# Kernel tuning notes

Hardware: AMD Instinct MI355X
Metric: run time of the kernel (lower is better)

## Reference

```python
import jax, jax.numpy as jnp
import numpy as np

CH = 256
HEADS = 4
RED = 8  # SE reduction on 2*CH channels


def _conv2d(x, w, pad):
    # x: [b,c,h,w], w: [o,i,kh,kw]
    return jax.lax.conv_general_dilated(
        x, w, window_strides=(1, 1), padding=[(pad, pad), (pad, pad)],
        dimension_numbers=('NCHW', 'OIHW', 'NCHW'))


def setup_inputs() -> dict:
    key = jax.random.key(0)
    ks = jax.random.split(key, 12)
    b, c, h, w = 4, CH, 64, 64
    c2 = 2 * c
    s = 0.02
    inp = {
        'color_feat': jax.random.normal(ks[0], (b, c, h, w), jnp.float32),
        'gray_feat': jax.random.normal(ks[1], (b, c, h, w), jnp.float32),
        'Wq': jax.random.normal(ks[2], (c, c), jnp.float32) * s,
        'Wk': jax.random.normal(ks[3], (c, c), jnp.float32) * s,
        'Wv': jax.random.normal(ks[4], (c, c), jnp.float32) * s,
        'Wproj': jax.random.normal(ks[5], (c, c), jnp.float32) * s,
        'ca_w1': jax.random.normal(ks[6], (c2 // RED, c2), jnp.float32) * s,
        'ca_w2': jax.random.normal(ks[7], (c2, c2 // RED), jnp.float32) * s,
        'sa_w': jax.random.normal(ks[8], (1, 2, 7, 7), jnp.float32) * s,
        'fuse_w': jax.random.normal(ks[9], (c, c2, 3, 3), jnp.float32) * s,
        'bn_gamma': jnp.ones((c,), jnp.float32),
        'bn_beta': jnp.zeros((c,), jnp.float32),
        'bn_mean': jnp.zeros((c,), jnp.float32),
        'bn_var': jnp.ones((c,), jnp.float32),
    }
    return inp


def reference(color_feat, gray_feat, Wq, Wk, Wv, Wproj, ca_w1, ca_w2,
              sa_w, fuse_w, bn_gamma, bn_beta, bn_mean, bn_var):
    b, c, h, w = color_feat.shape
    nh = HEADS
    d = c // nh
    scale = d ** -0.5

    def heads(x, W):
        # 1x1 conv then split heads: [b,c,h,w] -> [b,nh,hw,d]
        y = jnp.einsum('bchw,oc->bohw', x, W)
        return y.reshape(b, nh, d, h * w).transpose(0, 1, 3, 2)

    q = heads(color_feat, Wq)
    k = heads(gray_feat, Wk)
    v = heads(gray_feat, Wv)

    attn = jax.nn.softmax(jnp.einsum('bnid,bnjd->bnij', q, k) * scale, axis=-1)
    out = jnp.einsum('bnij,bnjd->bnid', attn, v)
    out = out.transpose(0, 1, 3, 2).reshape(b, c, h, w)
    out = jnp.einsum('bchw,oc->bohw', out, Wproj)

    cat = jnp.concatenate([out, gray_feat], axis=1)  # [b,2c,h,w]

    # Channel attention (SE with shared MLP on avg- and max-pooled vectors)
    def mlp(z):
        return jax.nn.relu(z @ ca_w1.T) @ ca_w2.T
    avg = cat.mean(axis=(2, 3))
    mx = cat.max(axis=(2, 3))
    wch = jax.nn.sigmoid(mlp(avg) + mlp(mx))[:, :, None, None]
    cat = cat * wch

    # Spatial attention: channel-mean/max -> 7x7 conv -> sigmoid gate
    sa_in = jnp.stack([cat.mean(axis=1), cat.max(axis=1)], axis=1)  # [b,2,h,w]
    wsp = jax.nn.sigmoid(_conv2d(sa_in, sa_w, pad=3))
    cat = cat * wsp

    # Fuse: 3x3 conv -> BatchNorm (inference stats) -> LeakyReLU(0.2)
    y = _conv2d(cat, fuse_w, pad=1)
    inv = bn_gamma / jnp.sqrt(bn_var + 1e-5)
    y = (y - bn_mean[None, :, None, None]) * inv[None, :, None, None] + bn_beta[None, :, None, None]
    return jnp.where(y > 0, y, 0.2 * y)
```

## Files before the change

### kernel.cpp

```cpp
#include <hip/hip_runtime.h>
#include <hip/hip_bf16.h>
#include <stdint.h>

#define HW_ 4096

typedef short bf16x8 __attribute__((ext_vector_type(8)));
typedef short short4v __attribute__((ext_vector_type(4)));
typedef short short8v __attribute__((ext_vector_type(8)));
typedef float f32x4 __attribute__((ext_vector_type(4)));
typedef float f32x16 __attribute__((ext_vector_type(16)));
typedef uint32_t u32x4 __attribute__((ext_vector_type(4)));

__device__ inline unsigned short f2bf(float x) {
  uint32_t u = __builtin_bit_cast(uint32_t, x);
  uint32_t r = ((u >> 16) & 1u) + 0x7fffu;
  return (unsigned short)((u + r) >> 16);
}
__device__ inline uint32_t cvt_pk_bf16(float lo, float hi) {
  uint32_t r;
  asm("v_cvt_pk_bf16_f32 %0, %1, %2" : "=v"(r) : "v"(lo), "v"(hi));
  return r;
}
__device__ inline float bf_lo(uint32_t u) { return __builtin_bit_cast(float, u << 16); }
__device__ inline float bf_hi(uint32_t u) { return __builtin_bit_cast(float, u & 0xffff0000u); }
__device__ inline void gld_lds16(const unsigned short* g, unsigned short* l) {
  __builtin_amdgcn_global_load_lds((const __attribute__((address_space(1))) void*)g,
                                   (__attribute__((address_space(3))) void*)l, 16, 0, 0);
}

__global__ __launch_bounds__(256) void xconv_kernel(
    const float* __restrict__ X, unsigned short* __restrict__ Y) {
  const int i = blockIdx.x * 256 + threadIdx.x;
  const int p = i & 4095;
  const int cg = (i >> 12) & 31;
  const int b = i >> 17;
  const float* src = X + ((size_t)b * 256 + cg * 8) * HW_ + p;
  float v[8];
#pragma unroll
  for (int e = 0; e < 8; ++e) v[e] = src[(size_t)e * HW_];
  uint4 o;
  o.x = cvt_pk_bf16(v[0], v[1]);
  o.y = cvt_pk_bf16(v[2], v[3]);
  o.z = cvt_pk_bf16(v[4], v[5]);
  o.w = cvt_pk_bf16(v[6], v[7]);
  *(uint4*)&Y[((size_t)(b * 32 + cg) * HW_ + p) * 8] = o;
}

__global__ __launch_bounds__(256) void prep_kernel(
    const float* __restrict__ Wq, const float* __restrict__ Wk,
    const float* __restrict__ Wv, const float* __restrict__ Wp,
    const float* __restrict__ fw,
    unsigned short* __restrict__ WqB, unsigned short* __restrict__ WkB,
    unsigned short* __restrict__ WvB, unsigned short* __restrict__ WpB,
    unsigned short* __restrict__ wt) {
  const int blk = blockIdx.x;
  if (blk < 128) {
    const int which = blk >> 5;
    const float* W = which == 0 ? Wq : which == 1 ? Wk : which == 2 ? Wv : Wp;
    unsigned short* Y = which == 0 ? WqB : which == 1 ? WkB : which == 2 ? WvB : WpB;
    const int i = (blk & 31) * 256 + threadIdx.x;
    const int o = i & 255;
    const int cg = i >> 8;
    float4 a = *(const float4*)&W[(size_t)o * 256 + cg * 8];
    float4 bq = *(const float4*)&W[(size_t)o * 256 + cg * 8 + 4];
    uint4 ov;
    ov.x = cvt_pk_bf16(a.x, a.y);
    ov.y = cvt_pk_bf16(a.z, a.w);
    ov.z = cvt_pk_bf16(bq.x, bq.y);
    ov.w = cvt_pk_bf16(bq.z, bq.w);
    *(uint4*)&Y[((size_t)cg * 256 + o) * 8] = ov;
  } else {
    const size_t i = (size_t)(blk - 128) * 256 + threadIdx.x;
    const int oc = (int)(i >> 9);
    const int ic = (int)(i & 511);
    const float* src = fw + i * 9;
#pragma unroll
    for (int tap = 0; tap < 9; ++tap)
      wt[((size_t)tap * 256 + oc) * 512 + ic] = f2bf(src[tap]);
  }
}

__global__ __launch_bounds__(256) void gemm_mfma_kernel(
    const unsigned short* __restrict__ Xbf, const unsigned short* __restrict__ Wbf,
    void* __restrict__ Yv, int mode, float oscale) {
  __shared__ unsigned short W_l[32][64][8];
  __shared__ unsigned short X_l[2][2][128][8];
  const int t = threadIdx.x;
  const int w = t >> 6;
  const int l = t & 63;
  const int n = l & 31;
  const int g32 = l >> 5;
  const int p0 = blockIdx.x * 128;
  const int o0 = blockIdx.y * 64;
  const int b = blockIdx.z;
  const int wo = w >> 1, wp = w & 1;
  const unsigned short* Xb = Xbf + (size_t)b * 32 * HW_ * 8;

  for (int i = t; i < 2048; i += 256) {
    const int ksg = i >> 6, oc = i & 63;
    gld_lds16(Wbf + ((size_t)ksg * 256 + o0 + oc) * 8, &W_l[0][0][0] + (size_t)i * 8);
  }
  {
    const int gg = t >> 7, pp = t & 127;
    gld_lds16(Xb + ((size_t)gg * HW_ + p0 + pp) * 8, &X_l[0][0][0][0] + (size_t)t * 8);
  }
  f32x16 acc[2] = {};
  int buf = 0;
  for (int ks = 0; ks < 16; ++ks) {
    asm volatile("s_waitcnt vmcnt(0)" ::: "memory");
    __syncthreads();
    if (ks < 15) {
      const int gg = t >> 7, pp = t & 127;
      gld_lds16(Xb + ((size_t)((ks + 1) * 2 + gg) * HW_ + p0 + pp) * 8,
                &X_l[buf ^ 1][0][0][0] + (size_t)t * 8);
    }
    bf16x8 af = *(const bf16x8*)&W_l[ks * 2 + g32][wo * 32 + n][0];
    bf16x8 b0 = *(const bf16x8*)&X_l[buf][g32][wp * 64 + n][0];
    bf16x8 b1 = *(const bf16x8*)&X_l[buf][g32][wp * 64 + 32 + n][0];
    acc[0] = __builtin_amdgcn_mfma_f32_32x32x16_bf16(af, b0, acc[0], 0, 0, 0);
    acc[1] = __builtin_amdgcn_mfma_f32_32x32x16_bf16(af, b1, acc[1], 0, 0, 0);
    buf ^= 1;
  }

  if (mode == 1) {
    unsigned short* Y = (unsigned short*)Yv;
    const size_t bh = (size_t)b * 4 + blockIdx.y;
#pragma unroll
    for (int pf = 0; pf < 2; ++pf) {
      const int p = p0 + wp * 64 + pf * 32 + n;
      unsigned short* dst = Y + (bh * HW_ + p) * 64 + wo * 32 + 4 * g32;
#pragma unroll
      for (int q = 0; q < 4; ++q) {
        uint2 uu;
        uu.x = cvt_pk_bf16(acc[pf][q * 4 + 0] * oscale, acc[pf][q * 4 + 1] * oscale);
        uu.y = cvt_pk_bf16(acc[pf][q * 4 + 2] * oscale, acc[pf][q * 4 + 3] * oscale);
        *(uint2*)&dst[8 * q] = uu;
      }
    }
  } else if (mode == 2) {
    unsigned short* Y = (unsigned short*)Yv;
#pragma unroll
    for (int pf = 0; pf < 2; ++pf) {
      const int p = p0 + wp * 64 + pf * 32 + n;
#pragma unroll
      for (int r = 0; r < 16; ++r) {
        const int m = (r & 3) + 8 * (r >> 2) + 4 * g32;
        Y[((size_t)b * 256 + o0 + wo * 32 + m) * HW_ + p] = f2bf(acc[pf][r]);
      }
    }
  } else {
    unsigned short* Y = (unsigned short*)Yv;
    const int cgb = (o0 + wo * 32) >> 3;
#pragma unroll
    for (int pf = 0; pf < 2; ++pf) {
      const int p = p0 + wp * 64 + pf * 32 + n;
#pragma unroll
      for (int q = 0; q < 4; ++q) {
        uint2 uu;
        uu.x = cvt_pk_bf16(acc[pf][q * 4 + 0], acc[pf][q * 4 + 1]);
        uu.y = cvt_pk_bf16(acc[pf][q * 4 + 2], acc[pf][q * 4 + 3]);
        *(uint2*)&Y[((size_t)(b * 32 + cgb + q) * HW_ + p) * 8 + 4 * g32] = uu;
      }
    }
  }
}

#define ATTN_STAGE(BUF, KP, VP)                                              \
  {                                                                          \
    gld_lds16((KP), &k_l[BUF][16 * w][0]);                                   \
    gld_lds16((KP) + (size_t)8 * 64, &k_l[BUF][16 * w + 8][0]);              \
    gld_lds16((VP), &v_l[BUF][16 * w][0]);                                   \
    gld_lds16((VP) + (size_t)8 * HW_, &v_l[BUF][16 * w + 8][0]);             \
  }

#define ATTN_COMPUTE(BUF)                                                    \
  {                                                                          \
    f32x4 accS[2][4];                                                        \
    _Pragma("unroll") for (int jt = 0; jt < 4; ++jt) {                       \
      const int jrow = jt * 16 + c;                                          \
      bf16x8 kf0 = *(const bf16x8*)&k_l[BUF][jrow][((0 + g) ^ (c & 7)) * 8]; \
      bf16x8 kf1 = *(const bf16x8*)&k_l[BUF][jrow][((4 + g) ^ (c & 7)) * 8]; \
      _Pragma("unroll") for (int qt = 0; qt < 2; ++qt) {                     \
        f32x4 s0 = __builtin_amdgcn_mfma_f32_16x16x32_bf16(kf0, qf[qt][0], zero4, 0, 0, 0); \
        accS[qt][jt] = __builtin_amdgcn_mfma_f32_16x16x32_bf16(kf1, qf[qt][1], s0, 0, 0, 0); \
      }                                                                      \
    }                                                                        \
    uint32_t pwu[2][2][4];                                                   \
    _Pragma("unroll") for (int qt = 0; qt < 2; ++qt) {                       \
      float rs = 0.f;                                                        \
      _Pragma("unroll") for (int jt = 0; jt < 4; ++jt) {                     \
        const float e0 = __builtin_amdgcn_exp2f(accS[qt][jt][0]);            \
        const float e1 = __builtin_amdgcn_exp2f(accS[qt][jt][1]);            \
        const float e2 = __builtin_amdgcn_exp2f(accS[qt][jt][2]);            \
        const float e3 = __builtin_amdgcn_exp2f(accS[qt][jt][3]);            \
        rs += (e0 + e1) + (e2 + e3);                                         \
        pwu[qt][jt >> 1][(jt & 1) * 2 + 0] = cvt_pk_bf16(e0, e1);            \
        pwu[qt][jt >> 1][(jt & 1) * 2 + 1] = cvt_pk_bf16(e2, e3);            \
      }                                                                      \
      l_r[qt] += rs;                                                         \
    }                                                                        \
    bf16x8 pf[2][2];                                                         \
    _Pragma("unroll") for (int qt = 0; qt < 2; ++qt)                         \
    _Pragma("unroll") for (int kb = 0; kb < 2; ++kb) {                       \
      u32x4 tmp = {pwu[qt][kb][0], pwu[qt][kb][1], pwu[qt][kb][2], pwu[qt][kb][3]}; \
      pf[qt][kb] = __builtin_bit_cast(bf16x8, tmp);                          \
    }                                                                        \
    _Pragma("unroll") for (int dt = 0; dt < 4; ++dt) {                       \
      const int row = dt * 16 + c;                                           \
      const int sw = c & 7;                                                  \
      _Pragma("unroll") for (int kb = 0; kb < 2; ++kb) {                     \
        union { short4v h[2]; bf16x8 v8; } vv;                               \
        vv.h[0] = *(const short4v*)&v_l[BUF][row][(((kb * 4 + 0) + (g >> 1)) ^ sw) * 8 + (g & 1) * 4]; \
        vv.h[1] = *(const short4v*)&v_l[BUF][row][(((kb * 4 + 2) + (g >> 1)) ^ sw) * 8 + (g & 1) * 4]; \
        accO[0][dt] = __builtin_amdgcn_mfma_f32_16x16x32_bf16(vv.v8, pf[0][kb], accO[0][dt], 0, 0, 0); \
        accO[1][dt] = __builtin_amdgcn_mfma_f32_16x16x32_bf16(vv.v8, pf[1][kb], accO[1][dt], 0, 0, 0); \
      }                                                                      \
    }                                                                        \
  }

__global__ __launch_bounds__(256) void attn_mfma_kernel(
    const unsigned short* __restrict__ Qb, const unsigned short* __restrict__ Kb,
    const unsigned short* __restrict__ Vb, unsigned short* __restrict__ Op0,
    unsigned short* __restrict__ Op1, float* __restrict__ lpart) {
  __shared__ unsigned short k_l[2][64][64];
  __shared__ unsigned short v_l[2][64][64];
  const int t = threadIdx.x;
  const int w = t >> 6;
  const int l = t & 63;
  const int g = l >> 4;
  const int c = l & 15;
  const int bid = blockIdx.x;
  const int gidx = (bid & 7) * 128 + (bid >> 3);
  const int bn = gidx >> 6;
  const int sq = gidx & 63;
  const int split = sq >> 5;
  const int q0 = (sq & 31) * 128 + w * 32;

  bf16x8 qf[2][2];
#pragma unroll
  for (int qt = 0; qt < 2; ++qt)
#pragma unroll
    for (int dh = 0; dh < 2; ++dh)
      qf[qt][dh] = *(const bf16x8*)&Qb[((size_t)bn * HW_ + q0 + qt * 16 + c) * 64 + dh * 32 + g * 8];

  const int srow = 16 * w + (l >> 3);
  const int schunk = (l & 7) ^ ((l >> 3) & 7);
  const unsigned short* gKp = Kb + ((size_t)bn * HW_ + split * 2048 + srow) * 64 + schunk * 8;
  const unsigned short* gVp = Vb + ((size_t)bn * 64 + srow) * HW_ + split * 2048 + schunk * 8;

  f32x4 accO[2][4] = {};
  float l_r[2] = {0.f, 0.f};
  const f32x4 zero4 = {0.f, 0.f, 0.f, 0.f};

  ATTN_STAGE(0, gKp, gVp);
  gKp += 4096; gVp += 64;

  for (int kt2 = 0; kt2 < 16; ++kt2) {
    asm volatile("s_waitcnt vmcnt(0)" ::: "memory");
    __syncthreads();
    ATTN_STAGE(1, gKp, gVp);
    gKp += 4096; gVp += 64;
    ATTN_COMPUTE(0)
    asm volatile("s_waitcnt vmcnt(0)" ::: "memory");
    __syncthreads();
    if (kt2 < 15) {
      ATTN_STAGE(0, gKp, gVp);
      gKp += 4096; gVp += 64;
    }
    ATTN_COMPUTE(1)
  }

  unsigned short* Op = split ? Op1 : Op0;
#pragma unroll
  for (int qt = 0; qt < 2; ++qt) {
    float s = l_r[qt];
    s += __shfl_xor(s, 16);
    s += __shfl_xor(s, 32);
    const int p = q0 + qt * 16 + c;
    if (l < 16) lpart[((size_t)split * 16 + bn) * HW_ + p] = s;
#pragma unroll
    for (int dt = 0; dt < 4; ++dt) {
      uint2 uu;
      uu.x = cvt_pk_bf16(accO[qt][dt][0], accO[qt][dt][1]);
      uu.y = cvt_pk_bf16(accO[qt][dt][2], accO[qt][dt][3]);
      *(uint2*)&Op[((size_t)bn * HW_ + p) * 64 + dt * 16 + g * 4] = uu;
    }
  }
}

__global__ __launch_bounds__(256) void attn_combine_kernel(
    const unsigned short* __restrict__ Op0, const unsigned short* __restrict__ Op1,
    const float* __restrict__ lpart, unsigned short* __restrict__ Abf) {
  const int tg = blockIdx.x * 256 + threadIdx.x;
  const int dg = tg & 7;
  const int q = (tg >> 3) & 4095;
  const int bn = tg >> 15;
  const size_t oidx = ((size_t)bn * HW_ + q) * 64 + dg * 8;
  uint4 a = *(const uint4*)&Op0[oidx];
  uint4 b2 = *(const uint4*)&Op1[oidx];
  const float lsum = lpart[(size_t)bn * HW_ + q] + lpart[(size_t)(16 + bn) * HW_ + q];
  const float inv = 1.0f / lsum;
  const uint32_t ua[4] = {a.x, a.y, a.z, a.w};
  const uint32_t ub[4] = {b2.x, b2.y, b2.z, b2.w};
  uint32_t o[4];
#pragma unroll
  for (int k = 0; k < 4; ++k) {
    const float lo = (bf_lo(ua[k]) + bf_lo(ub[k])) * inv;
    const float hi = (bf_hi(ua[k]) + bf_hi(ub[k])) * inv;
    o[k] = cvt_pk_bf16(lo, hi);
  }
  const int head = bn & 3, bb = bn >> 2;
  const int cg = head * 8 + dg;
  uint4 ov = {o[0], o[1], o[2], o[3]};
  *(uint4*)&Abf[((size_t)(bb * 32 + cg) * HW_ + q) * 8] = ov;
}

__global__ __launch_bounds__(256) void pool_kernel(
    const unsigned short* __restrict__ Pbf, const unsigned short* __restrict__ Gbf,
    float* __restrict__ psum, float* __restrict__ pmaxH) {
  const int cg = blockIdx.x;
  const int b = blockIdx.y;
  const int half = blockIdx.z;
  const int t = threadIdx.x;
  const unsigned short* P = Pbf + ((size_t)(b * 32 + cg) * HW_ + half * 2048) * 8;
  const unsigned short* G = Gbf + ((size_t)(b * 32 + cg) * HW_ + half * 2048) * 8;
  float s[16], m[16];
#pragma unroll
  for (int i = 0; i < 16; ++i) { s[i] = 0.f; m[i] = -1e30f; }
  for (int p = t; p < 2048; p += 256) {
    uint4 a = *(const uint4*)&P[(size_t)p * 8];
    uint4 gg = *(const uint4*)&G[(size_t)p * 8];
    const uint32_t ua[4] = {a.x, a.y, a.z, a.w};
    const uint32_t ug[4] = {gg.x, gg.y, gg.z, gg.w};
#pragma unroll
    for (int q = 0; q < 4; ++q) {
      const float a0 = bf_lo(ua[q]), a1 = bf_hi(ua[q]);
      const float g0 = bf_lo(ug[q]), g1 = bf_hi(ug[q]);
      s[q * 2] += a0; s[q * 2 + 1] += a1;
      m[q * 2] = fmaxf(m[q * 2], a0); m[q * 2 + 1] = fmaxf(m[q * 2 + 1], a1);
      s[8 + q * 2] += g0; s[8 + q * 2 + 1] += g1;
      m[8 + q * 2] = fmaxf(m[8 + q * 2], g0); m[8 + q * 2 + 1] = fmaxf(m[8 + q * 2 + 1], g1);
    }
  }
#pragma unroll
  for (int i = 0; i < 16; ++i)
#pragma unroll
    for (int off = 1; off < 64; off <<= 1) {
      s[i] += __shfl_xor(s[i], off);
      m[i] = fmaxf(m[i], __shfl_xor(m[i], off));
    }
  __shared__ float red[4][32];
  const int wv = t >> 6;
  if ((t & 63) == 0) {
#pragma unroll
    for (int i = 0; i < 16; ++i) { red[wv][i] = s[i]; red[wv][16 + i] = m[i]; }
  }
  __syncthreads();
  if (t < 32) {
    const float v0 = red[0][t], v1 = red[1][t], v2 = red[2][t], v3 = red[3][t];
    if (t < 16) {
      const int ch = (t < 8) ? cg * 8 + t : 256 + cg * 8 + (t - 8);
      psum[half * 2048 + b * 512 + ch] = v0 + v1 + v2 + v3;
    } else {
      const int i = t - 16;
      const int ch = (i < 8) ? cg * 8 + i : 256 + cg * 8 + (i - 8);
      pmaxH[half * 2048 + b * 512 + ch] = fmaxf(fmaxf(v0, v1), fmaxf(v2, v3));
    }
  }
}

__global__ __launch_bounds__(256) void se_kernel(
    const float* __restrict__ psum, const float* __restrict__ pmaxH,
    const float* __restrict__ w1, const float* __restrict__ w2,
    float* __restrict__ wch) {
  const int b = blockIdx.x;
  const int t = threadIdx.x;
  __shared__ float za[512], zm[512], hs[64];
  za[t] = (psum[b * 512 + t] + psum[2048 + b * 512 + t]) * (1.f / 4096.f);
  za[256 + t] = (psum[b * 512 + 256 + t] + psum[2048 + b * 512 + 256 + t]) * (1.f / 4096.f);
  zm[t] = fmaxf(pmaxH[b * 512 + t], pmaxH[2048 + b * 512 + t]);
  zm[256 + t] = fmaxf(pmaxH[b * 512 + 256 + t], pmaxH[2048 + b * 512 + 256 + t]);
  __syncthreads();
  if (t < 64) {
    float ha = 0.f, hm = 0.f;
    for (int c = 0; c < 512; ++c) {
      const float w = w1[t * 512 + c];
      ha += w * za[c];
      hm += w * zm[c];
    }
    hs[t] = fmaxf(ha, 0.f) + fmaxf(hm, 0.f);
  }
  __syncthreads();
  for (int o = t; o < 512; o += 256) {
    float acc = 0.f;
#pragma unroll
    for (int hh = 0; hh < 64; ++hh) acc += hs[hh] * w2[o * 64 + hh];
    wch[b * 512 + o] = 1.f / (1.f + __expf(-acc));
  }
}

__global__ __launch_bounds__(256) void sa_reduce_kernel(
    const unsigned short* __restrict__ Pbf, const unsigned short* __restrict__ Gbf,
    const float* __restrict__ wch, float* __restrict__ sa_in) {
  const int b = blockIdx.y;
  const int t = threadIdx.x;
  const int px = t & 63;
  const int sl = t >> 6;
  const int p = blockIdx.x * 64 + px;
  __shared__ float wl[512];
  __shared__ float sred[4][64], mred[4][64];
  wl[t] = wch[b * 512 + t];
  wl[256 + t] = wch[b * 512 + 256 + t];
  __syncthreads();
  float s = 0.f, mx = -1e30f;
#pragma unroll 4
  for (int k = 0; k < 16; ++k) {
    const int chunk = sl * 16 + k;
    const unsigned short* src = (chunk < 32)
        ? &Pbf[((size_t)(b * 32 + chunk) * HW_ + p) * 8]
        : &Gbf[((size_t)(b * 32 + (chunk - 32)) * HW_ + p) * 8];
    uint4 a = *(const uint4*)src;
    const uint32_t u[4] = {a.x, a.y, a.z, a.w};
#pragma unroll
    for (int q = 0; q < 4; ++q) {
      const float v0 = bf_lo(u[q]) * wl[chunk * 8 + q * 2];
      const float v1 = bf_hi(u[q]) * wl[chunk * 8 + q * 2 + 1];
      s += v0 + v1;
      mx = fmaxf(mx, fmaxf(v0, v1));
    }
  }
  sred[sl][px] = s;
  mred[sl][px] = mx;
  __syncthreads();
  if (sl == 0) {
    const float S = sred[0][px] + sred[1][px] + sred[2][px] + sred[3][px];
    const float M = fmaxf(fmaxf(mred[0][px], mred[1][px]), fmaxf(mred[2][px], mred[3][px]));
    sa_in[((size_t)b * 2 + 0) * HW_ + p] = S * (1.f / 512.f);
    sa_in[((size_t)b * 2 + 1) * HW_ + p] = M;
  }
}

__global__ __launch_bounds__(256) void sa_conv_kernel(
    const float* __restrict__ sa_in, const float* __restrict__ sa_w,
    float* __restrict__ wsp) {
  const int b = blockIdx.y;
  const int t = threadIdx.x;
  __shared__ float pl[2][64][64];
  __shared__ float wl[98];
  for (int e = t; e < 8192; e += 256) ((float*)pl)[e] = sa_in[(size_t)b * 8192 + e];
  if (t < 98) wl[t] = sa_w[t];
  __syncthreads();
  const int pix = blockIdx.x * 256 + t;
  const int y = pix >> 6, x = pix & 63;
  float acc = 0.f;
#pragma unroll
  for (int ic = 0; ic < 2; ++ic)
#pragma unroll
    for (int ky = 0; ky < 7; ++ky) {
      const int yy = y + ky - 3;
      if (yy < 0 || yy > 63) continue;
#pragma unroll
      for (int kx = 0; kx < 7; ++kx) {
        const int xx = x + kx - 3;
        if (xx < 0 || xx > 63) continue;
        acc += pl[ic][yy][xx] * wl[ic * 49 + ky * 7 + kx];
      }
    }
  wsp[(size_t)b * HW_ + pix] = 1.f / (1.f + __expf(-acc));
}

__global__ __launch_bounds__(256) void gate_kernel(
    const unsigned short* __restrict__ Pbf, const unsigned short* __restrict__ Gbf,
    const float* __restrict__ wch, const float* __restrict__ wsp,
    unsigned short* __restrict__ catg) {
  const int yp = blockIdx.x;
  const int b = blockIdx.y;
  const int t = threadIdx.x;
  unsigned short* rowp = catg + ((size_t)b * 66 + yp) * 80 * 512;
  if (yp == 0 || yp == 65) {
    short8v z = {};
    for (int m = t; m < 5120; m += 256) *(short8v*)&rowp[m * 8] = z;
    return;
  }
  const int y = yp - 1;
  __shared__ unsigned short tile[64][512];
  __shared__ float wchl[512];
  __shared__ float wspl[64];
  for (int e = t; e < 512; e += 256) wchl[e] = wch[b * 512 + e];
  if (t < 64) wspl[t] = wsp[(size_t)b * HW_ + y * 64 + t];
  {
    short8v z = {};
    for (int m = t; m < 1024; m += 256) {
      const int col = m >> 6;
      const int xi = (col < 8) ? col : (col + 64);
      *(short8v*)&rowp[(size_t)xi * 512 + (m & 63) * 8] = z;
    }
  }
  __syncthreads();
  const int x = t & 63;
  const int cs = t >> 6;
  const float wx = wspl[x];
#pragma unroll
  for (int k = 0; k < 16; ++k) {
    const int chunk = cs * 16 + k;
    const unsigned short* src = (chunk < 32)
        ? &Pbf[((size_t)(b * 32 + chunk) * HW_ + y * 64 + x) * 8]
        : &Gbf[((size_t)(b * 32 + (chunk - 32)) * HW_ + y * 64 + x) * 8];
    uint4 a = *(const uint4*)src;
    const uint32_t u[4] = {a.x, a.y, a.z, a.w};
    uint32_t o[4];
#pragma unroll
    for (int q = 0; q < 4; ++q) {
      const float lo = bf_lo(u[q]) * wchl[chunk * 8 + q * 2] * wx;
      const float hi = bf_hi(u[q]) * wchl[chunk * 8 + q * 2 + 1] * wx;
      o[q] = cvt_pk_bf16(lo, hi);
    }
    uint4 ov = {o[0], o[1], o[2], o[3]};
    *(uint4*)&tile[x][(chunk ^ (x & 7)) * 8] = ov;
  }
  __syncthreads();
#pragma unroll
  for (int j = 0; j < 16; ++j) {
    const int xi = (t >> 6) + 4 * j;
    const int c8 = t & 63;
    uint4 v = *(const uint4*)&tile[xi][(c8 ^ (xi & 7)) * 8];
    *(uint4*)&rowp[(size_t)(xi + 8) * 512 + c8 * 8] = v;
  }
}

__global__ __launch_bounds__(256) void fuse_mfma_kernel(
    const unsigned short* __restrict__ catg, const unsigned short* __restrict__ wt,
    const float* __restrict__ bn_g, const float* __restrict__ bn_b,
    const float* __restrict__ bn_m, const float* __restrict__ bn_v,
    float* __restrict__ out) {
  __shared__ unsigned short X_l[2][6][2][80][8];
  __shared__ unsigned short W_l[2][9][2][32][8];
  __shared__ float invl[32], shl[32];
  const int t = threadIdx.x;
  const int w = t >> 6;
  const int l = t & 63;
  const int n = l & 31;
  const int g = l >> 5;
  const int i = blockIdx.x;
  const int xcd = i & 7, slot = i >> 3;
  const int ocB = slot & 7;
  const int yb = xcd + 8 * (slot >> 3);
  const int y0 = (yb & 15) * 4;
  const int o0 = ocB * 32;
  const int b = yb >> 4;

  if (t < 32) {
    const float iv = bn_g[o0 + t] * rsqrtf(bn_v[o0 + t] + 1e-5f);
    invl[t] = iv;
    shl[t] = bn_b[o0 + t] - bn_m[o0 + t] * iv;
  }

  const unsigned short* catb = catg + ((size_t)b * 66 + y0) * 80 * 512;

  auto stageX = [&](int bi, int ic0) {
    for (int wc = w; wc < 15; wc += 4) {
      const int m = wc * 64 + l;
      const int lr = m / 160;
      const int rem = m - lr * 160;
      const int half = rem / 80;
      const int xi = rem - half * 80;
      gld_lds16(catb + ((size_t)lr * 80 + xi) * 512 + ic0 + half * 8,
                &X_l[bi][0][0][0][0] + (size_t)wc * 512);
    }
  };
  auto stageW = [&](int bi, int ic0) {
    for (int wc = w; wc < 9; wc += 4) {
      const int m = wc * 64 + l;
      const int tap = m >> 6;
      const int rem = m & 63;
      const int half = rem >> 5;
      const int oc = rem & 31;
      gld_lds16(wt + ((size_t)tap * 256 + o0 + oc) * 512 + ic0 + half * 8,
                &W_l[bi][0][0][0][0] + (size_t)wc * 512);
    }
  };

  f32x16 acc[2] = {};

  stageX(0, 0);
  stageW(0, 0);
  int buf = 0;
  for (int ks = 0; ks < 32; ++ks) {
    asm volatile("s_waitcnt vmcnt(0)" ::: "memory");
    __syncthreads();
    if (ks < 31) {
      stageX(buf ^ 1, (ks + 1) * 16);
      stageW(buf ^ 1, (ks + 1) * 16);
    }
#pragma unroll
    for (int ky = 0; ky < 3; ++ky) {
      const int lr = w + ky;
#pragma unroll
      for (int kx = 0; kx < 3; ++kx) {
        const int tap = ky * 3 + kx;
        bf16x8 a0 = *(const bf16x8*)&W_l[buf][tap][g][n][0];
        bf16x8 b0 = *(const bf16x8*)&X_l[buf][lr][g][n + kx + 7][0];
        bf16x8 b1 = *(const bf16x8*)&X_l[buf][lr][g][32 + n + kx + 7][0];
        acc[0] = __builtin_amdgcn_mfma_f32_32x32x16_bf16(a0, b0, acc[0], 0, 0, 0);
        acc[1] = __builtin_amdgcn_mfma_f32_32x32x16_bf16(a0, b1, acc[1], 0, 0, 0);
      }
    }
    buf ^= 1;
  }

#pragma unroll
  for (int pf = 0; pf < 2; ++pf)
#pragma unroll
    for (int r = 0; r < 16; ++r) {
      const int row = (r & 3) + 8 * (r >> 2) + 4 * g;
      const float yv = acc[pf][r] * invl[row] + shl[row];
      const float ov = yv > 0.f ? yv : 0.2f * yv;
      out[((size_t)b * 256 + o0 + row) * HW_ + (size_t)(y0 + w) * 64 + pf * 32 + n] = ov;
    }
}

extern "C" void kernel_launch(void* const* d_in, const int* in_sizes, int n_in,
                              void* d_out, int out_size, void* d_ws, size_t ws_size,
                              hipStream_t stream) {
  const float* color  = (const float*)d_in[0];
  const float* gray   = (const float*)d_in[1];
  const float* Wq     = (const float*)d_in[2];
  const float* Wk     = (const float*)d_in[3];
  const float* Wv     = (const float*)d_in[4];
  const float* Wproj  = (const float*)d_in[5];
  const float* ca_w1  = (const float*)d_in[6];
  const float* ca_w2  = (const float*)d_in[7];
  const float* sa_w   = (const float*)d_in[8];
  const float* fuse_w = (const float*)d_in[9];
  const float* bn_g   = (const float*)d_in[10];
  const float* bn_b   = (const float*)d_in[11];
  const float* bn_m   = (const float*)d_in[12];
  const float* bn_v   = (const float*)d_in[13];
  float* out = (float*)d_out;

  char* ws = (char*)d_ws;
  unsigned short* Cbf = (unsigned short*)(ws);
  unsigned short* Gbf = (unsigned short*)(ws + (8u << 20));
  unsigned short* Qbf = (unsigned short*)(ws + (16u << 20));
  unsigned short* Kbf = (unsigned short*)(ws + (24u << 20));
  unsigned short* Vbf = (unsigned short*)(ws + (32u << 20));
  unsigned short* Abf = (unsigned short*)(ws + (16u << 20));
  unsigned short* Pbf = (unsigned short*)(ws);
  unsigned short* Op0 = (unsigned short*)(ws);
  unsigned short* Op1 = (unsigned short*)(ws + (48u << 20));
  float* lpart        = (float*)(ws + (56u << 20));
  unsigned short* catg = (unsigned short*)(ws + (24u << 20));
  unsigned short* WqB = (unsigned short*)(ws + (45u << 20));
  unsigned short* WkB = WqB + 65536;
  unsigned short* WvB = WkB + 65536;
  unsigned short* WpB = WvB + 65536;
  unsigned short* Wt  = (unsigned short*)(ws + (45u << 20) + (1u << 19));
  float* psum  = (float*)(ws + (57u << 20));
  float* pmaxH = psum + 4096;
  float* wch   = pmaxH + 4096;
  float* sa_in = wch + 2048;
  float* wsp   = sa_in + 32768;
  (void)in_sizes; (void)n_in; (void)out_size; (void)ws_size;

  const float qscale = 0.125f * 1.44269504f;

  prep_kernel<<<dim3(640), 256, 0, stream>>>(Wq, Wk, Wv, Wproj, fuse_w,
                                             WqB, WkB, WvB, WpB, Wt);
  xconv_kernel<<<dim3(2048), 256, 0, stream>>>(color, Cbf);
  xconv_kernel<<<dim3(2048), 256, 0, stream>>>(gray, Gbf);

  dim3 g_gemm(32, 4, 4);
  gemm_mfma_kernel<<<g_gemm, 256, 0, stream>>>(Cbf, WqB, Qbf, 1, qscale);
  gemm_mfma_kernel<<<g_gemm, 256, 0, stream>>>(Gbf, WkB, Kbf, 1, 1.0f);
  gemm_mfma_kernel<<<g_gemm, 256, 0, stream>>>(Gbf, WvB, Vbf, 2, 1.0f);
  attn_mfma_kernel<<<dim3(1024), 256, 0, stream>>>(Qbf, Kbf, Vbf, Op0, Op1, lpart);
  attn_combine_kernel<<<dim3(2048), 256, 0, stream>>>(Op0, Op1, lpart, Abf);
  gemm_mfma_kernel<<<g_gemm, 256, 0, stream>>>(Abf, WpB, Pbf, 3, 1.0f);

  pool_kernel<<<dim3(32, 4, 2), 256, 0, stream>>>(Pbf, Gbf, psum, pmaxH);
  se_kernel<<<dim3(4), 256, 0, stream>>>(psum, pmaxH, ca_w1, ca_w2, wch);
  sa_reduce_kernel<<<dim3(64, 4), 256, 0, stream>>>(Pbf, Gbf, wch, sa_in);
  sa_conv_kernel<<<dim3(16, 4), 256, 0, stream>>>(sa_in, sa_w, wsp);
  gate_kernel<<<dim3(66, 4), 256, 0, stream>>>(Pbf, Gbf, wch, wsp, catg);
  fuse_mfma_kernel<<<dim3(512), 256, 0, stream>>>(catg, Wt, bn_g, bn_b, bn_m, bn_v, out);
}
```

Measured before the change: 267.5 us.

## Drop attention KV split, use 4-stage LDS pipeline and fuse normalization into epilogue

The attention kernel no longer splits the key range in two, so the separate combine kernel and its partial-output and row-sum buffers go away. Normalization and the head-to-channel-group layout write now happen in the attention epilogue. The LDS K/V staging grows from double to quadruple buffering with partial vmcnt waits, to keep loads in flight across two tiles, and LDS offsets are precomputed. The trade-off is half as many blocks (512 instead of 1024), each running twice as many iterations, plus higher LDS use per block, which could lower occupancy.

```diff
diff --git a/kernel.cpp b/kernel.cpp
--- a/kernel.cpp
+++ b/kernel.cpp
@@ -165,21 +165,22 @@
   }
 }
 
-#define ATTN_STAGE(BUF, KP, VP)                                              \
+#define ATTN_STAGE(SB)                                                       \
   {                                                                          \
-    gld_lds16((KP), &k_l[BUF][16 * w][0]);                                   \
-    gld_lds16((KP) + (size_t)8 * 64, &k_l[BUF][16 * w + 8][0]);              \
-    gld_lds16((VP), &v_l[BUF][16 * w][0]);                                   \
-    gld_lds16((VP) + (size_t)8 * HW_, &v_l[BUF][16 * w + 8][0]);             \
+    gld_lds16(gKp, kst + (SB) * 4096);                                       \
+    gld_lds16(gKp + 8 * 64, kst + (SB) * 4096 + 512);                        \
+    gld_lds16(gVp, vst + (SB) * 4096);                                       \
+    gld_lds16(gVp + (size_t)8 * HW_, vst + (SB) * 4096 + 512);               \
+    gKp += 4096;                                                             \
+    gVp += 64;                                                               \
   }
 
 #define ATTN_COMPUTE(BUF)                                                    \
   {                                                                          \
     f32x4 accS[2][4];                                                        \
     _Pragma("unroll") for (int jt = 0; jt < 4; ++jt) {                       \
-      const int jrow = jt * 16 + c;                                          \
-      bf16x8 kf0 = *(const bf16x8*)&k_l[BUF][jrow][((0 + g) ^ (c & 7)) * 8]; \
-      bf16x8 kf1 = *(const bf16x8*)&k_l[BUF][jrow][((4 + g) ^ (c & 7)) * 8]; \
+      bf16x8 kf0 = *(const bf16x8*)&k_l[(BUF) * 4096 + jt * 1024 + ko0];     \
+      bf16x8 kf1 = *(const bf16x8*)&k_l[(BUF) * 4096 + jt * 1024 + ko1];     \
       _Pragma("unroll") for (int qt = 0; qt < 2; ++qt) {                     \
         f32x4 s0 = __builtin_amdgcn_mfma_f32_16x16x32_bf16(kf0, qf[qt][0], zero4, 0, 0, 0); \
         accS[qt][jt] = __builtin_amdgcn_mfma_f32_16x16x32_bf16(kf1, qf[qt][1], s0, 0, 0, 0); \
@@ -206,35 +207,38 @@
       pf[qt][kb] = __builtin_bit_cast(bf16x8, tmp);                          \
     }                                                                        \
     _Pragma("unroll") for (int dt = 0; dt < 4; ++dt) {                       \
-      const int row = dt * 16 + c;                                           \
-      const int sw = c & 7;                                                  \
-      _Pragma("unroll") for (int kb = 0; kb < 2; ++kb) {                     \
-        union { short4v h[2]; bf16x8 v8; } vv;                               \
-        vv.h[0] = *(const short4v*)&v_l[BUF][row][(((kb * 4 + 0) + (g >> 1)) ^ sw) * 8 + (g & 1) * 4]; \
-        vv.h[1] = *(const short4v*)&v_l[BUF][row][(((kb * 4 + 2) + (g >> 1)) ^ sw) * 8 + (g & 1) * 4]; \
-        accO[0][dt] = __builtin_amdgcn_mfma_f32_16x16x32_bf16(vv.v8, pf[0][kb], accO[0][dt], 0, 0, 0); \
-        accO[1][dt] = __builtin_amdgcn_mfma_f32_16x16x32_bf16(vv.v8, pf[1][kb], accO[1][dt], 0, 0, 0); \
-      }                                                                      \
+      union { short4v h[2]; bf16x8 v8; } vv0, vv1;                           \
+      vv0.h[0] = *(const short4v*)&v_l[(BUF) * 4096 + dt * 1024 + vo00];     \
+      vv0.h[1] = *(const short4v*)&v_l[(BUF) * 4096 + dt * 1024 + vo01];     \
+      vv1.h[0] = *(const short4v*)&v_l[(BUF) * 4096 + dt * 1024 + vo10];     \
+      vv1.h[1] = *(const short4v*)&v_l[(BUF) * 4096 + dt * 1024 + vo11];     \
+      accO[0][dt] = __builtin_amdgcn_mfma_f32_16x16x32_bf16(vv0.v8, pf[0][0], accO[0][dt], 0, 0, 0); \
+      accO[1][dt] = __builtin_amdgcn_mfma_f32_16x16x32_bf16(vv0.v8, pf[1][0], accO[1][dt], 0, 0, 0); \
+      accO[0][dt] = __builtin_amdgcn_mfma_f32_16x16x32_bf16(vv1.v8, pf[0][1], accO[0][dt], 0, 0, 0); \
+      accO[1][dt] = __builtin_amdgcn_mfma_f32_16x16x32_bf16(vv1.v8, pf[1][1], accO[1][dt], 0, 0, 0); \
     }                                                                        \
   }
+
+#define ATTN_PHASE(B, SB, VMSTR, DOST)                                       \
+  asm volatile("s_waitcnt " VMSTR ::: "memory");                             \
+  __builtin_amdgcn_s_barrier();                                              \
+  if (DOST) { ATTN_STAGE(SB) }                                               \
+  ATTN_COMPUTE(B)
 
 __global__ __launch_bounds__(256) void attn_mfma_kernel(
     const unsigned short* __restrict__ Qb, const unsigned short* __restrict__ Kb,
-    const unsigned short* __restrict__ Vb, unsigned short* __restrict__ Op0,
-    unsigned short* __restrict__ Op1, float* __restrict__ lpart) {
-  __shared__ unsigned short k_l[2][64][64];
-  __shared__ unsigned short v_l[2][64][64];
+    const unsigned short* __restrict__ Vb, unsigned short* __restrict__ Abf) {
+  __shared__ unsigned short k_l[4 * 4096];
+  __shared__ unsigned short v_l[4 * 4096];
   const int t = threadIdx.x;
   const int w = t >> 6;
   const int l = t & 63;
   const int g = l >> 4;
   const int c = l & 15;
   const int bid = blockIdx.x;
-  const int gidx = (bid & 7) * 128 + (bid >> 3);
-  const int bn = gidx >> 6;
-  const int sq = gidx & 63;
-  const int split = sq >> 5;
-  const int q0 = (sq & 31) * 128 + w * 32;
+  const int gidx = (bid & 7) * 64 + (bid >> 3);
+  const int bn = gidx >> 5;
+  const int q0 = (gidx & 31) * 128 + w * 32;
 
   bf16x8 qf[2][2];
 #pragma unroll
@@ -243,76 +247,59 @@
     for (int dh = 0; dh < 2; ++dh)
       qf[qt][dh] = *(const bf16x8*)&Qb[((size_t)bn * HW_ + q0 + qt * 16 + c) * 64 + dh * 32 + g * 8];
 
+  const int sw = c & 7;
+  const int ko0 = c * 64 + ((g ^ sw) * 8);
+  const int ko1 = c * 64 + (((4 + g) ^ sw) * 8);
+  const int vb_ = c * 64 + (g & 1) * 4;
+  const int gh = g >> 1;
+  const int vo00 = vb_ + (((0 + gh) ^ sw) * 8);
+  const int vo01 = vb_ + (((2 + gh) ^ sw) * 8);
+  const int vo10 = vb_ + (((4 + gh) ^ sw) * 8);
+  const int vo11 = vb_ + (((6 + gh) ^ sw) * 8);
+
   const int srow = 16 * w + (l >> 3);
   const int schunk = (l & 7) ^ ((l >> 3) & 7);
-  const unsigned short* gKp = Kb + ((size_t)bn * HW_ + split * 2048 + srow) * 64 + schunk * 8;
-  const unsigned short* gVp = Vb + ((size_t)bn * 64 + srow) * HW_ + split * 2048 + schunk * 8;
+  const unsigned short* gKp = Kb + ((size_t)bn * HW_ + srow) * 64 + schunk * 8;
+  const unsigned short* gVp = Vb + ((size_t)bn * 64 + srow) * HW_ + schunk * 8;
+  unsigned short* kst = k_l + w * 1024;
+  unsigned short* vst = v_l + w * 1024;
 
   f32x4 accO[2][4] = {};
   float l_r[2] = {0.f, 0.f};
   const f32x4 zero4 = {0.f, 0.f, 0.f, 0.f};
 
-  ATTN_STAGE(0, gKp, gVp);
-  gKp += 4096; gVp += 64;
-
-  for (int kt2 = 0; kt2 < 16; ++kt2) {
-    asm volatile("s_waitcnt vmcnt(0)" ::: "memory");
-    __syncthreads();
-    ATTN_STAGE(1, gKp, gVp);
-    gKp += 4096; gVp += 64;
-    ATTN_COMPUTE(0)
-    asm volatile("s_waitcnt vmcnt(0)" ::: "memory");
-    __syncthreads();
-    if (kt2 < 15) {
-      ATTN_STAGE(0, gKp, gVp);
-      gKp += 4096; gVp += 64;
-    }
-    ATTN_COMPUTE(1)
-  }
-
-  unsigned short* Op = split ? Op1 : Op0;
+  ATTN_STAGE(0)
+  ATTN_STAGE(1)
+
+  for (int t4 = 0; t4 < 15; ++t4) {
+    ATTN_PHASE(0, 2, "vmcnt(4)", 1)
+    ATTN_PHASE(1, 3, "vmcnt(4)", 1)
+    ATTN_PHASE(2, 0, "vmcnt(4)", 1)
+    ATTN_PHASE(3, 1, "vmcnt(4)", 1)
+  }
+  ATTN_PHASE(0, 2, "vmcnt(4)", 1)
+  ATTN_PHASE(1, 3, "vmcnt(4)", 1)
+  ATTN_PHASE(2, 0, "vmcnt(4)", 0)
+  ATTN_PHASE(3, 0, "vmcnt(0)", 0)
+
+  const int head = bn & 3;
+  const int bb = bn >> 2;
 #pragma unroll
   for (int qt = 0; qt < 2; ++qt) {
     float s = l_r[qt];
     s += __shfl_xor(s, 16);
     s += __shfl_xor(s, 32);
+    const float inv = 1.0f / s;
     const int p = q0 + qt * 16 + c;
-    if (l < 16) lpart[((size_t)split * 16 + bn) * HW_ + p] = s;
 #pragma unroll
     for (int dt = 0; dt < 4; ++dt) {
       uint2 uu;
-      uu.x = cvt_pk_bf16(accO[qt][dt][0], accO[qt][dt][1]);
-      uu.y = cvt_pk_bf16(accO[qt][dt][2], accO[qt][dt][3]);
-      *(uint2*)&Op[((size_t)bn * HW_ + p) * 64 + dt * 16 + g * 4] = uu;
-    }
-  }
-}
-
-__global__ __launch_bounds__(256) void attn_combine_kernel(
-    const unsigned short* __restrict__ Op0, const unsigned short* __restrict__ Op1,
-    const float* __restrict__ lpart, unsigned short* __restrict__ Abf) {
-  const int tg = blockIdx.x * 256 + threadIdx.x;
-  const int dg = tg & 7;
-  const int q = (tg >> 3) & 4095;
-  const int bn = tg >> 15;
-  const size_t oidx = ((size_t)bn * HW_ + q) * 64 + dg * 8;
-  uint4 a = *(const uint4*)&Op0[oidx];
-  uint4 b2 = *(const uint4*)&Op1[oidx];
-  const float lsum = lpart[(size_t)bn * HW_ + q] + lpart[(size_t)(16 + bn) * HW_ + q];
-  const float inv = 1.0f / lsum;
-  const uint32_t ua[4] = {a.x, a.y, a.z, a.w};
-  const uint32_t ub[4] = {b2.x, b2.y, b2.z, b2.w};
-  uint32_t o[4];
-#pragma unroll
-  for (int k = 0; k < 4; ++k) {
-    const float lo = (bf_lo(ua[k]) + bf_lo(ub[k])) * inv;
-    const float hi = (bf_hi(ua[k]) + bf_hi(ub[k])) * inv;
-    o[k] = cvt_pk_bf16(lo, hi);
-  }
-  const int head = bn & 3, bb = bn >> 2;
-  const int cg = head * 8 + dg;
-  uint4 ov = {o[0], o[1], o[2], o[3]};
-  *(uint4*)&Abf[((size_t)(bb * 32 + cg) * HW_ + q) * 8] = ov;
+      uu.x = cvt_pk_bf16(accO[qt][dt][0] * inv, accO[qt][dt][1] * inv);
+      uu.y = cvt_pk_bf16(accO[qt][dt][2] * inv, accO[qt][dt][3] * inv);
+      const int cg = head * 8 + dt * 2 + (g >> 1);
+      *(uint2*)&Abf[((size_t)(bb * 32 + cg) * HW_ + p) * 8 + (g & 1) * 4] = uu;
+    }
+  }
 }
 
 __global__ __launch_bounds__(256) void pool_kernel(
@@ -644,18 +631,15 @@
   unsigned short* Qbf = (unsigned short*)(ws + (16u << 20));
   unsigned short* Kbf = (unsigned short*)(ws + (24u << 20));
   unsigned short* Vbf = (unsigned short*)(ws + (32u << 20));
-  unsigned short* Abf = (unsigned short*)(ws + (16u << 20));
-  unsigned short* Pbf = (unsigned short*)(ws);
-  unsigned short* Op0 = (unsigned short*)(ws);
-  unsigned short* Op1 = (unsigned short*)(ws + (48u << 20));
-  float* lpart        = (float*)(ws + (56u << 20));
+  unsigned short* Abf = (unsigned short*)(ws);
+  unsigned short* Pbf = (unsigned short*)(ws + (16u << 20));
   unsigned short* catg = (unsigned short*)(ws + (24u << 20));
   unsigned short* WqB = (unsigned short*)(ws + (45u << 20));
   unsigned short* WkB = WqB + 65536;
   unsigned short* WvB = WkB + 65536;
   unsigned short* WpB = WvB + 65536;
   unsigned short* Wt  = (unsigned short*)(ws + (45u << 20) + (1u << 19));
-  float* psum  = (float*)(ws + (57u << 20));
+  float* psum  = (float*)(ws + (48u << 20));
   float* pmaxH = psum + 4096;
   float* wch   = pmaxH + 4096;
   float* sa_in = wch + 2048;
@@ -673,8 +657,7 @@
   gemm_mfma_kernel<<<g_gemm, 256, 0, stream>>>(Cbf, WqB, Qbf, 1, qscale);
   gemm_mfma_kernel<<<g_gemm, 256, 0, stream>>>(Gbf, WkB, Kbf, 1, 1.0f);
   gemm_mfma_kernel<<<g_gemm, 256, 0, stream>>>(Gbf, WvB, Vbf, 2, 1.0f);
-  attn_mfma_kernel<<<dim3(1024), 256, 0, stream>>>(Qbf, Kbf, Vbf, Op0, Op1, lpart);
-  attn_combine_kernel<<<dim3(2048), 256, 0, stream>>>(Op0, Op1, lpart, Abf);
+  attn_mfma_kernel<<<dim3(512), 256, 0, stream>>>(Qbf, Kbf, Vbf, Abf);
   gemm_mfma_kernel<<<g_gemm, 256, 0, stream>>>(Abf, WpB, Pbf, 3, 1.0f);
 
   pool_kernel<<<dim3(32, 4, 2), 256, 0, stream>>>(Pbf, Gbf, psum, pmaxH);
```

New measurement: 253.4 us. -5.3%, faster.
